# Optimization experiments

Hardware: AMD Instinct MI355X
Metric: run time of the kernel (lower is better)

## Reference

```python
import jax, jax.numpy as jnp
import numpy as np

N_EMBD = 1024
HEAD_SIZE = 64
BATCH = 4
T = 4096  # == block_size


def setup_inputs() -> dict:
    key = jax.random.key(0)
    kx, kq, kk, kv = jax.random.split(key, 4)
    x = jax.random.normal(kx, (BATCH, T, N_EMBD), dtype=jnp.float32)
    Wq = jax.random.normal(kq, (N_EMBD, HEAD_SIZE), dtype=jnp.float32) * 0.02
    Wk = jax.random.normal(kk, (N_EMBD, HEAD_SIZE), dtype=jnp.float32) * 0.02
    Wv = jax.random.normal(kv, (N_EMBD, HEAD_SIZE), dtype=jnp.float32) * 0.02
    return {"x": x, "Wq": Wq, "Wk": Wk, "Wv": Wv}


def reference(x, Wq, Wk, Wv):
    # x: [B, T, C]; projections: [B, T, H]
    B, Tlen, C = x.shape
    q = jnp.einsum('btc,ch->bth', x, Wq)
    k = jnp.einsum('btc,ch->bth', x, Wk)
    v = jnp.einsum('btc,ch->bth', x, Wv)
    # NOTE: original scales by C**-0.5 where C = n_embd (input channels), not head_size
    scale = jnp.asarray(C, x.dtype) ** -0.5
    wei = jnp.einsum('bth,bsh->bts', q, k) * scale  # [B, T, T]
    causal = jnp.tril(jnp.ones((Tlen, Tlen), dtype=bool))
    wei = jnp.where(causal, wei, -jnp.inf)
    wei = jax.nn.softmax(wei, axis=-1)
    # dropout p=0.0 -> identity
    out = jnp.einsum('bts,bsh->bth', wei, v)  # [B, T, H]
    return out
```

## Files before the change

kernel.cpp:

```cpp
#include <hip/hip_runtime.h>
#include <math.h>

#define T_SEQ 4096
#define NBATCH 4
#define NEMBD 1024
#define HS 64
#define BT (NBATCH * T_SEQ)

typedef float f32x4 __attribute__((ext_vector_type(4)));
typedef short s8v  __attribute__((ext_vector_type(8)));
typedef short s4v  __attribute__((ext_vector_type(4)));

__device__ __forceinline__ short f2b_rne(float f) {
    union { float f; unsigned u; } v; v.f = f;
    unsigned r = v.u + 0x7fffu + ((v.u >> 16) & 1u);
    return (short)(r >> 16);
}
__device__ __forceinline__ unsigned pk2(float lo, float hi) {
    return __builtin_amdgcn_perm(__float_as_uint(hi), __float_as_uint(lo), 0x07060302u);
}

__global__ __launch_bounds__(256) void wtrans_kernel(
        const float* __restrict__ Wq, const float* __restrict__ Wk,
        const float* __restrict__ Wv, short* __restrict__ Wt) {
    int e = blockIdx.x * 256 + threadIdx.x;
    int col = e & 63, k = (e >> 6) & 1023, mat = e >> 16;
    const float* W = (mat == 0) ? Wq : ((mat == 1) ? Wk : Wv);
    float scale = (mat == 0) ? 0.0450842298f : 1.0f;
    Wt[(size_t)(mat * 64 + col) * 1024 + k] = f2b_rne(W[k * 64 + col] * scale);
}

template<bool SRC_BF16>
__global__ __launch_bounds__(512) void proj_kernel(
        const void* __restrict__ xsrc, const short* __restrict__ Wt,
        short* __restrict__ QKV) {
    __shared__ short xs[32 * 72];
    __shared__ short wsh[192 * 72];
    int tid = threadIdx.x;
    int w = tid >> 6, l = tid & 63, quad = l >> 4, c16 = l & 15;
    int rt = w >> 2, cg = w & 3;
    int row0 = blockIdx.x * 32;
    short* VpT = QKV + 2 * (size_t)BT * HS;

    const short* xb = (const short*)xsrc;
    const float* xf = (const float*)xsrc;
    int xrow_b = tid >> 3,  xc8 = (tid & 7) * 8;
    int xrow_f = tid >> 4,  xc4 = (tid & 15) * 4;

    s8v  wreg[3];
    s8v  xreg_b;
    float4 xreg_f;
    #pragma unroll
    for (int i = 0; i < 3; i++) {
        int c = tid + 512 * i;
        wreg[i] = *(const s8v*)(Wt + (size_t)(c >> 3) * 1024 + ((c & 7) * 8));
    }
    if (SRC_BF16) {
        if (tid < 256) xreg_b = *(const s8v*)(xb + (size_t)(row0 + xrow_b) * 1024 + xc8);
    } else {
        xreg_f = *(const float4*)(xf + (size_t)(row0 + xrow_f) * 1024 + xc4);
    }

    f32x4 acc[3] = {};
    for (int ko = 0; ko < NEMBD; ko += 64) {
        #pragma unroll
        for (int i = 0; i < 3; i++) {
            int c = tid + 512 * i;
            *(s8v*)(wsh + (c >> 3) * 72 + ((c & 7) * 8)) = wreg[i];
        }
        if (SRC_BF16) {
            if (tid < 256) *(s8v*)(xs + xrow_b * 72 + xc8) = xreg_b;
        } else {
            union { s4v v; unsigned u[2]; } pkv;
            pkv.u[0] = pk2(xreg_f.x, xreg_f.y);
            pkv.u[1] = pk2(xreg_f.z, xreg_f.w);
            *(s4v*)(xs + xrow_f * 72 + xc4) = pkv.v;
        }
        __syncthreads();
        {
            int kn = (ko + 64 < NEMBD) ? (ko + 64) : 0;
            #pragma unroll
            for (int i = 0; i < 3; i++) {
                int c = tid + 512 * i;
                wreg[i] = *(const s8v*)(Wt + (size_t)(c >> 3) * 1024 + kn + ((c & 7) * 8));
            }
            if (SRC_BF16) {
                if (tid < 256) xreg_b = *(const s8v*)(xb + (size_t)(row0 + xrow_b) * 1024 + kn + xc8);
            } else {
                xreg_f = *(const float4*)(xf + (size_t)(row0 + xrow_f) * 1024 + kn + xc4);
            }
        }
        #pragma unroll
        for (int ks = 0; ks < 2; ks++) {
            s8v a = *(const s8v*)(xs + (rt * 16 + c16) * 72 + ks * 32 + quad * 8);
            #pragma unroll
            for (int j = 0; j < 3; j++) {
                s8v b = *(const s8v*)(wsh + (cg * 48 + j * 16 + c16) * 72 + ks * 32 + quad * 8);
                acc[j] = __builtin_amdgcn_mfma_f32_16x16x32_bf16(a, b, acc[j], 0, 0, 0);
            }
        }
        __syncthreads();
    }
    #pragma unroll
    for (int j = 0; j < 3; j++) {
        int g = cg * 48 + j * 16 + c16;
        int mat = g >> 6, h = g & 63;
        if (mat < 2) {
            #pragma unroll
            for (int r = 0; r < 4; r++) {
                int row = row0 + rt * 16 + quad * 4 + r;
                QKV[(size_t)mat * BT * HS + (size_t)row * HS + h] = f2b_rne(acc[j][r]);
            }
        } else {
            int tg = row0 + rt * 16 + quad * 4;
            int b = tg >> 12, t = tg & 4095;
            size_t base = (((size_t)((b * 64 + (t >> 6)) * 64 + h)) << 6) + (t & 63);
            s4v pv;
            #pragma unroll
            for (int r = 0; r < 4; r++) pv[r] = f2b_rne(acc[j][r]);
            *(s4v*)(VpT + base) = pv;
        }
    }
}

__global__ __launch_bounds__(512, 4) void attn_kernel(
        const short* __restrict__ QKV, float* __restrict__ out) {
    __shared__ float smem[9216];
    short* Ps = (short*)smem;

    int tid = threadIdx.x;
    int w = tid >> 6, l = tid & 63, quad = l >> 4, c16 = l & 15;
    int bi = blockIdx.x;
    int b  = (bi & 7) >> 1;
    int r8 = bi >> 3;
    int p  = bi & 1;
    int jt = (r8 < 32) ? (127 - (2 * r8 + p)) : (2 * (r8 - 32) + p);
    int q0 = jt * 32;

    const short* Qp  = QKV;
    const short* Kp  = QKV + (size_t)BT * HS;
    const short* VpT = QKV + 2 * (size_t)BT * HS;
    size_t bT = (size_t)b * T_SEQ;

    s8v qf[2][2];
    #pragma unroll
    for (int qt = 0; qt < 2; qt++)
        #pragma unroll
        for (int h = 0; h < 2; h++)
            qf[qt][h] = *(const s8v*)(Qp + (bT + q0 + qt * 16 + c16) * HS + h * 32 + quad * 8);

    f32x4 o[2][4] = {};
    float lsum[2] = {0.f, 0.f};
    int nkt = (q0 >> 6) + 1;
    short* Pw[2] = { Ps + (w * 2) * 1152, Ps + (w * 2 + 1) * 1152 };
    const short* kbase = Kp + (bT + c16) * HS + quad * 8;
    const short* vbase = VpT + (((size_t)((b * 64) * 64 + c16)) << 6) + quad * 8;

    for (int kt = w; kt < nkt; kt += 8) {
        int kb = kt * 64;
        bool last = (kt == nkt - 1);

        s8v kf[4][2];
        #pragma unroll
        for (int nt = 0; nt < 4; nt++) {
            const short* kr = kbase + (size_t)(kb + nt * 16) * HS;
            kf[nt][0] = *(const s8v*)kr;
            kf[nt][1] = *(const s8v*)(kr + 32);
        }
        f32x4 st[2][4];
        #pragma unroll
        for (int nt = 0; nt < 4; nt++) {
            f32x4 z0 = {0.f, 0.f, 0.f, 0.f}, z1 = {0.f, 0.f, 0.f, 0.f};
            z0 = __builtin_amdgcn_mfma_f32_16x16x32_bf16(kf[nt][0], qf[0][0], z0, 0, 0, 0);
            z0 = __builtin_amdgcn_mfma_f32_16x16x32_bf16(kf[nt][1], qf[0][1], z0, 0, 0, 0);
            z1 = __builtin_amdgcn_mfma_f32_16x16x32_bf16(kf[nt][0], qf[1][0], z1, 0, 0, 0);
            z1 = __builtin_amdgcn_mfma_f32_16x16x32_bf16(kf[nt][1], qf[1][1], z1, 0, 0, 0);
            st[0][nt] = z0; st[1][nt] = z1;
        }
        s8v vf[4][2];
        #pragma unroll
        for (int nt = 0; nt < 4; nt++) {
            const short* vr = vbase + (((size_t)(kt * 64 + nt * 16)) << 6);
            vf[nt][0] = *(const s8v*)vr;
            vf[nt][1] = *(const s8v*)(vr + 32);
        }
        #pragma unroll
        for (int qt = 0; qt < 2; qt++) {
            int qrow = q0 + qt * 16 + c16;
            #pragma unroll
            for (int nt = 0; nt < 4; nt++) {
                float pr[4];
                #pragma unroll
                for (int rr = 0; rr < 4; rr++) {
                    float v = st[qt][nt][rr];
                    if (last && (kb + nt * 16 + quad * 4 + rr > qrow)) v = -30000.f;
                    pr[rr] = __builtin_amdgcn_exp2f(v);
                    lsum[qt] += pr[rr];
                }
                union { s4v v; unsigned u[2]; } pkv;
                pkv.u[0] = pk2(pr[0], pr[1]); pkv.u[1] = pk2(pr[2], pr[3]);
                *(s4v*)(Pw[qt] + c16 * 72 + nt * 16 + quad * 4) = pkv.v;
            }
        }
        s8v pa[2][2];
        #pragma unroll
        for (int qt = 0; qt < 2; qt++) {
            pa[qt][0] = *(const s8v*)(Pw[qt] + c16 * 72 + quad * 8);
            pa[qt][1] = *(const s8v*)(Pw[qt] + c16 * 72 + quad * 8 + 32);
        }
        #pragma unroll
        for (int nt = 0; nt < 4; nt++)
            #pragma unroll
            for (int qt = 0; qt < 2; qt++) {
                o[qt][nt] = __builtin_amdgcn_mfma_f32_16x16x32_bf16(pa[qt][0], vf[nt][0], o[qt][nt], 0, 0, 0);
                o[qt][nt] = __builtin_amdgcn_mfma_f32_16x16x32_bf16(pa[qt][1], vf[nt][1], o[qt][nt], 0, 0, 0);
            }
    }

    #pragma unroll
    for (int qt = 0; qt < 2; qt++) {
        lsum[qt] += __shfl_xor(lsum[qt], 16);
        lsum[qt] += __shfl_xor(lsum[qt], 32);
    }

    #pragma unroll
    for (int qt = 0; qt < 2; qt++) {
        __syncthreads();
        #pragma unroll
        for (int nt = 0; nt < 4; nt++)
            *(f32x4*)(smem + ((w * 4 + nt) * 64 + l) * 4) = o[qt][nt];
        if (l < 16) smem[8192 + w * 16 + l] = lsum[qt];
        __syncthreads();
        if (w < 4) {
            f32x4 os = {0.f, 0.f, 0.f, 0.f}, ls = {0.f, 0.f, 0.f, 0.f};
            #pragma unroll
            for (int s = 0; s < 8; s++) {
                os += *(const f32x4*)(smem + ((s * 4 + w) * 64 + l) * 4);
                ls += *(const f32x4*)(smem + 8192 + s * 16 + quad * 4);
            }
            #pragma unroll
            for (int rr = 0; rr < 4; rr++)
                out[(bT + q0 + qt * 16 + quad * 4 + rr) * HS + w * 16 + c16] = os[rr] / ls[rr];
        }
    }
}

extern "C" void kernel_launch(void* const* d_in, const int* in_sizes, int n_in,
                              void* d_out, int out_size, void* d_ws, size_t ws_size,
                              hipStream_t stream) {
    const float* x  = (const float*)d_in[0];
    const float* Wq = (const float*)d_in[1];
    const float* Wk = (const float*)d_in[2];
    const float* Wv = (const float*)d_in[3];
    float* out = (float*)d_out;

    short* QKV = (short*)d_ws;
    short* Wt  = QKV + (size_t)3 * BT * HS;

    wtrans_kernel<<<768, 256, 0, stream>>>(Wq, Wk, Wv, Wt);
    proj_kernel<false><<<BT / 32, 512, 0, stream>>>(x, Wt, QKV);
    attn_kernel<<<512, 512, 0, stream>>>(QKV, out);
}
```

Baseline: 153.1 us.

## Load projection weights directly into registers and double-buffer x tile in LDS

The projection kernel no longer stages the 192x64 weight tile through shared memory. Each wave loads its MFMA B operands straight from global memory into registers with a ping-pong register prefetch. The x tile is double-buffered in LDS, so each 64-wide K step needs only one barrier instead of two. This removes LDS traffic and synchronisation for the weights, at the cost of more registers and redundant global (L2) weight reads across the two row-tile waves.

```diff
diff --git a/kernel.cpp b/kernel.cpp
--- a/kernel.cpp
+++ b/kernel.cpp
@@ -30,77 +30,95 @@
     Wt[(size_t)(mat * 64 + col) * 1024 + k] = f2b_rne(W[k * 64 + col] * scale);
 }
 
-template<bool SRC_BF16>
 __global__ __launch_bounds__(512) void proj_kernel(
-        const void* __restrict__ xsrc, const short* __restrict__ Wt,
+        const float* __restrict__ xf, const short* __restrict__ Wt,
         short* __restrict__ QKV) {
-    __shared__ short xs[32 * 72];
-    __shared__ short wsh[192 * 72];
+    __shared__ short xs[2][32 * 72];
     int tid = threadIdx.x;
     int w = tid >> 6, l = tid & 63, quad = l >> 4, c16 = l & 15;
     int rt = w >> 2, cg = w & 3;
     int row0 = blockIdx.x * 32;
     short* VpT = QKV + 2 * (size_t)BT * HS;
 
-    const short* xb = (const short*)xsrc;
-    const float* xf = (const float*)xsrc;
-    int xrow_b = tid >> 3,  xc8 = (tid & 7) * 8;
-    int xrow_f = tid >> 4,  xc4 = (tid & 15) * 4;
-
-    s8v  wreg[3];
-    s8v  xreg_b;
-    float4 xreg_f;
-    #pragma unroll
-    for (int i = 0; i < 3; i++) {
-        int c = tid + 512 * i;
-        wreg[i] = *(const s8v*)(Wt + (size_t)(c >> 3) * 1024 + ((c & 7) * 8));
-    }
-    if (SRC_BF16) {
-        if (tid < 256) xreg_b = *(const s8v*)(xb + (size_t)(row0 + xrow_b) * 1024 + xc8);
-    } else {
-        xreg_f = *(const float4*)(xf + (size_t)(row0 + xrow_f) * 1024 + xc4);
-    }
+    int xrow = tid >> 4, xc4 = (tid & 15) * 4;
+    const float* xp = xf + (size_t)(row0 + xrow) * 1024 + xc4;
+    const short* wp0 = Wt + (size_t)(cg * 48 +  0 + c16) * 1024 + quad * 8;
+    const short* wp1 = Wt + (size_t)(cg * 48 + 16 + c16) * 1024 + quad * 8;
+    const short* wp2 = Wt + (size_t)(cg * 48 + 32 + c16) * 1024 + quad * 8;
+
+    float4 xreg = *(const float4*)xp;
+    {
+        union { s4v v; unsigned u[2]; } pkv;
+        pkv.u[0] = pk2(xreg.x, xreg.y);
+        pkv.u[1] = pk2(xreg.z, xreg.w);
+        *(s4v*)(&xs[0][xrow * 72 + xc4]) = pkv.v;
+    }
+    s8v bA[3][2], bB[3][2];
+    #pragma unroll
+    for (int ks = 0; ks < 2; ks++) {
+        bA[0][ks] = *(const s8v*)(wp0 + ks * 32);
+        bA[1][ks] = *(const s8v*)(wp1 + ks * 32);
+        bA[2][ks] = *(const s8v*)(wp2 + ks * 32);
+    }
+    xreg = *(const float4*)(xp + 64);
+    __syncthreads();
 
     f32x4 acc[3] = {};
-    for (int ko = 0; ko < NEMBD; ko += 64) {
-        #pragma unroll
-        for (int i = 0; i < 3; i++) {
-            int c = tid + 512 * i;
-            *(s8v*)(wsh + (c >> 3) * 72 + ((c & 7) * 8)) = wreg[i];
-        }
-        if (SRC_BF16) {
-            if (tid < 256) *(s8v*)(xs + xrow_b * 72 + xc8) = xreg_b;
-        } else {
-            union { s4v v; unsigned u[2]; } pkv;
-            pkv.u[0] = pk2(xreg_f.x, xreg_f.y);
-            pkv.u[1] = pk2(xreg_f.z, xreg_f.w);
-            *(s4v*)(xs + xrow_f * 72 + xc4) = pkv.v;
-        }
-        __syncthreads();
+    #pragma unroll
+    for (int sp = 0; sp < 8; sp++) {
+        const int ko = sp * 128;
         {
-            int kn = (ko + 64 < NEMBD) ? (ko + 64) : 0;
-            #pragma unroll
-            for (int i = 0; i < 3; i++) {
-                int c = tid + 512 * i;
-                wreg[i] = *(const s8v*)(Wt + (size_t)(c >> 3) * 1024 + kn + ((c & 7) * 8));
-            }
-            if (SRC_BF16) {
-                if (tid < 256) xreg_b = *(const s8v*)(xb + (size_t)(row0 + xrow_b) * 1024 + kn + xc8);
-            } else {
-                xreg_f = *(const float4*)(xf + (size_t)(row0 + xrow_f) * 1024 + kn + xc4);
-            }
-        }
-        #pragma unroll
-        for (int ks = 0; ks < 2; ks++) {
-            s8v a = *(const s8v*)(xs + (rt * 16 + c16) * 72 + ks * 32 + quad * 8);
-            #pragma unroll
-            for (int j = 0; j < 3; j++) {
-                s8v b = *(const s8v*)(wsh + (cg * 48 + j * 16 + c16) * 72 + ks * 32 + quad * 8);
-                acc[j] = __builtin_amdgcn_mfma_f32_16x16x32_bf16(a, b, acc[j], 0, 0, 0);
-            }
-        }
-        __syncthreads();
-    }
+            const int kn = ko + 64;
+            #pragma unroll
+            for (int ks = 0; ks < 2; ks++) {
+                bB[0][ks] = *(const s8v*)(wp0 + kn + ks * 32);
+                bB[1][ks] = *(const s8v*)(wp1 + kn + ks * 32);
+                bB[2][ks] = *(const s8v*)(wp2 + kn + ks * 32);
+            }
+            {
+                union { s4v v; unsigned u[2]; } pkv;
+                pkv.u[0] = pk2(xreg.x, xreg.y);
+                pkv.u[1] = pk2(xreg.z, xreg.w);
+                *(s4v*)(&xs[1][xrow * 72 + xc4]) = pkv.v;
+            }
+            const int kx = (kn + 64 < NEMBD) ? kn + 64 : 0;
+            xreg = *(const float4*)(xp + kx);
+            #pragma unroll
+            for (int ks = 0; ks < 2; ks++) {
+                s8v a = *(const s8v*)(&xs[0][(rt * 16 + c16) * 72 + ks * 32 + quad * 8]);
+                acc[0] = __builtin_amdgcn_mfma_f32_16x16x32_bf16(a, bA[0][ks], acc[0], 0, 0, 0);
+                acc[1] = __builtin_amdgcn_mfma_f32_16x16x32_bf16(a, bA[1][ks], acc[1], 0, 0, 0);
+                acc[2] = __builtin_amdgcn_mfma_f32_16x16x32_bf16(a, bA[2][ks], acc[2], 0, 0, 0);
+            }
+            __syncthreads();
+        }
+        {
+            const int kn = (ko + 128 < NEMBD) ? ko + 128 : 0;
+            #pragma unroll
+            for (int ks = 0; ks < 2; ks++) {
+                bA[0][ks] = *(const s8v*)(wp0 + kn + ks * 32);
+                bA[1][ks] = *(const s8v*)(wp1 + kn + ks * 32);
+                bA[2][ks] = *(const s8v*)(wp2 + kn + ks * 32);
+            }
+            {
+                union { s4v v; unsigned u[2]; } pkv;
+                pkv.u[0] = pk2(xreg.x, xreg.y);
+                pkv.u[1] = pk2(xreg.z, xreg.w);
+                *(s4v*)(&xs[0][xrow * 72 + xc4]) = pkv.v;
+            }
+            const int kx = (ko + 192 < NEMBD) ? ko + 192 : 0;
+            xreg = *(const float4*)(xp + kx);
+            #pragma unroll
+            for (int ks = 0; ks < 2; ks++) {
+                s8v a = *(const s8v*)(&xs[1][(rt * 16 + c16) * 72 + ks * 32 + quad * 8]);
+                acc[0] = __builtin_amdgcn_mfma_f32_16x16x32_bf16(a, bB[0][ks], acc[0], 0, 0, 0);
+                acc[1] = __builtin_amdgcn_mfma_f32_16x16x32_bf16(a, bB[1][ks], acc[1], 0, 0, 0);
+                acc[2] = __builtin_amdgcn_mfma_f32_16x16x32_bf16(a, bB[2][ks], acc[2], 0, 0, 0);
+            }
+            __syncthreads();
+        }
+    }
+
     #pragma unroll
     for (int j = 0; j < 3; j++) {
         int g = cg * 48 + j * 16 + c16;
@@ -258,6 +276,6 @@
     short* Wt  = QKV + (size_t)3 * BT * HS;
 
     wtrans_kernel<<<768, 256, 0, stream>>>(Wq, Wk, Wv, Wt);
-    proj_kernel<false><<<BT / 32, 512, 0, stream>>>(x, Wt, QKV);
+    proj_kernel<<<BT / 32, 512, 0, stream>>>(x, Wt, QKV);
     attn_kernel<<<512, 512, 0, stream>>>(QKV, out);
 }
```

Result: slower. 175.6 us (+14.7%).
